# Optimization experiments

Measured on AMD Instinct MI355X. Metric: run time of the kernel, lower is better.

Reference implementation:

```python
import jax, jax.numpy as jnp
import numpy as np

MAX_POS = 100
N_NEGS = 10
B, L = 64, 100
VOCAB, WDIM, PDIM = 100000, 300, 50
N_TYPES, TDIM = 5000, 128
N_RELS, EDIM = 500, 128
N_FILTERS, FILTER_SIZES, EN_DIM = 128, (3, 5, 7), 512
N_POSS_C = 10
N_CANDS = N_POSS_C + N_NEGS
NB_PER_CAND = 64
N_NB = B * N_CANDS * NB_PER_CAND          # 81920 neighbor rows
TYPES_PER_NB = 4
T_TOTAL = N_NB * TYPES_PER_NB             # 327680 type entries
DIM = WDIM + PDIM                         # conv input width
CTX_DIM = len(FILTER_SIZES) * N_FILTERS * 2
EN_HID1 = CTX_DIM + EDIM                  # 896
NEG_INF = 1e10


def setup_inputs() -> dict:
    key = jax.random.key(0)
    ks = jax.random.split(key, 20)
    tokens = jax.random.randint(ks[0], (B, L), 0, VOCAB)
    pos_wrt_m = jax.random.randint(ks[1], (B, L), 0, 2 * MAX_POS + 1) - MAX_POS
    masks = jnp.ones((B, L), jnp.float32)
    nb_types = jax.random.randint(ks[2], (T_TOTAL,), 0, N_TYPES)
    nb_type_ids = jnp.arange(T_TOTAL) // TYPES_PER_NB      # each nb row gets TYPES_PER_NB types
    nb_n_types = jnp.full((N_NB,), TYPES_PER_NB, jnp.int32)
    nb_rs = jax.random.randint(ks[3], (N_NB,), 0, N_RELS)
    cand_nb_ids = jnp.arange(N_NB) // NB_PER_CAND          # each candidate gets NB_PER_CAND nbs
    real_n_poss = jax.random.randint(ks[4], (B,), 1, N_POSS_C + 1)
    we = jax.random.normal(ks[5], (VOCAB, WDIM), jnp.float32)
    word_embs = we / jnp.linalg.norm(we, axis=1, keepdims=True)  # F.normalize
    pos_emb_table = jax.random.normal(ks[6], (2 * MAX_POS + 1, PDIM), jnp.float32)
    type_emb_table = jax.random.normal(ks[7], (N_TYPES, TDIM), jnp.float32)
    rel_emb_table = jax.random.normal(ks[8], (N_RELS, EDIM), jnp.float32)
    rel_weight = jax.random.normal(ks[9], (TDIM, EDIM), jnp.float32) * np.sqrt(2.0 / EDIM)  # kaiming fan_out
    convs = {}
    for i, fs in enumerate(FILTER_SIZES):
        convs[f'conv_w{fs}'] = jax.random.normal(ks[10 + i], (N_FILTERS, 1, fs, DIM), jnp.float32) * np.sqrt(1.0 / (fs * DIM))
        convs[f'conv_b{fs}'] = jnp.zeros((N_FILTERS,), jnp.float32)
    scorer_W1 = jax.random.normal(ks[13], (EN_HID1, EN_DIM), jnp.float32) * np.sqrt(1.0 / EN_HID1)
    scorer_b1 = jnp.zeros((EN_DIM,), jnp.float32)
    scorer_W2 = jax.random.normal(ks[14], (EN_DIM, 1), jnp.float32) * np.sqrt(1.0 / EN_DIM)
    scorer_b2 = jnp.zeros((1,), jnp.float32)
    noise_W1 = jax.random.normal(ks[15], (EN_HID1, EN_DIM), jnp.float32) * np.sqrt(1.0 / EN_HID1)
    noise_b1 = jnp.zeros((EN_DIM,), jnp.float32)
    noise_W2 = jax.random.normal(ks[16], (EN_DIM, 1), jnp.float32) * np.sqrt(1.0 / EN_DIM)
    noise_b2 = jnp.zeros((1,), jnp.float32)
    return dict(tokens=tokens, pos_wrt_m=pos_wrt_m, masks=masks, nb_types=nb_types,
                nb_type_ids=nb_type_ids, nb_n_types=nb_n_types, nb_rs=nb_rs,
                cand_nb_ids=cand_nb_ids, real_n_poss=real_n_poss, n_poss=N_POSS_C,
                word_embs=word_embs, pos_emb_table=pos_emb_table,
                type_emb_table=type_emb_table, rel_emb_table=rel_emb_table,
                rel_weight=rel_weight, **convs,
                scorer_W1=scorer_W1, scorer_b1=scorer_b1, scorer_W2=scorer_W2, scorer_b2=scorer_b2,
                noise_W1=noise_W1, noise_b1=noise_b1, noise_W2=noise_W2, noise_b2=noise_b2)


def _mlp(x, W1, b1, W2, b2):
    return jax.nn.relu(x @ W1 + b1) @ W2 + b2


def _conv(x, w, b, fs):
    # x: [B,1,L,DIM], w: [nf,1,fs,DIM] -> [B,nf,L] (odd fs, 'same' padding on length)
    y = jax.lax.conv_general_dilated(x, w, window_strides=(1, 1),
                                     padding=[(fs // 2, fs // 2), (0, 0)],
                                     dimension_numbers=('NCHW', 'OIHW', 'NCHW'))
    return jax.nn.relu(y + b[None, :, None, None])[:, :, :, 0]


def _forward(tokens, pos_wrt_m, masks, nb_types, nb_type_ids, nb_n_types, nb_rs,
             cand_nb_ids, real_n_poss, n_poss, word_embs, pos_emb_table,
             type_emb_table, rel_emb_table, rel_weight,
             conv_w3, conv_b3, conv_w5, conv_b5, conv_w7, conv_b7,
             scorer_W1, scorer_b1, scorer_W2, scorer_b2,
             noise_W1, noise_b1, noise_W2, noise_b2):
    n_cands = n_poss + N_NEGS
    # --- neighbor type aggregation (TYPE_OPT == 'mean') ---
    nb_embs = jax.ops.segment_sum(type_emb_table[nb_types], nb_type_ids, num_segments=N_NB)
    nb_embs = nb_embs / nb_n_types[:, None].astype(jnp.float32)
    # --- relation transform + scatter_add into candidates ---
    msg = nb_embs @ rel_weight + rel_emb_table[nb_rs]                 # [N_NB, EDIM]
    cand_embs = jax.nn.relu(jax.ops.segment_sum(msg, cand_nb_ids, num_segments=B * n_cands))
    # --- PCNN context encoder ---
    pos_ment = pos_emb_table[pos_wrt_m + MAX_POS]                     # [B,L,PDIM]
    inp = jnp.concatenate([word_embs[tokens], pos_ment], axis=2)      # [B,L,DIM]
    x = inp[:, None, :, :]                                            # [B,1,L,DIM]
    conved = [_conv(x, conv_w3, conv_b3, 3), _conv(x, conv_w5, conv_b5, 5), _conv(x, conv_w7, conv_b7, 7)]
    ml = (pos_wrt_m <= 0).astype(jnp.float32)[:, None, :]             # [B,1,L]
    mr = ((pos_wrt_m >= 0).astype(jnp.float32) * masks)[:, None, :]
    pooled_l = jnp.concatenate([jnp.max(c * ml - (1.0 - ml) * NEG_INF, axis=2) for c in conved], axis=1)
    pooled_r = jnp.concatenate([jnp.max(c * mr - (1.0 - mr) * NEG_INF, axis=2) for c in conved], axis=1)
    ctx_vecs = jnp.concatenate([pooled_l, pooled_r], axis=1)          # [B, CTX_DIM]
    # --- scorer over (ctx, cand) pairs ---
    rp_ctx = jnp.broadcast_to(ctx_vecs[:, None, :], (B, n_cands, CTX_DIM)).reshape(B * n_cands, CTX_DIM)
    reprs = jnp.concatenate([rp_ctx, cand_embs], axis=1)
    scores = _mlp(reprs, scorer_W1, scorer_b1, scorer_W2, scorer_b2).reshape(B, n_cands)
    pos_mask = jnp.arange(1, n_poss + 1)[None, :] <= real_n_poss[:, None]
    mask = jnp.concatenate([pos_mask, jnp.ones((B, N_NEGS), bool)], axis=1)
    scores = jnp.where(mask, scores, -NEG_INF)
    # --- noise scorer over softmax-weighted positive candidate embedding ---
    p = jax.nn.softmax(scores[:, :n_poss], axis=-1)
    e = jnp.sum(cand_embs.reshape(B, n_cands, EDIM)[:, :n_poss, :] * p[:, :, None], axis=1)
    noise_scores = _mlp(jnp.concatenate([ctx_vecs, e], axis=1), noise_W1, noise_b1, noise_W2, noise_b2)
    return scores, noise_scores


def reference(tokens, pos_wrt_m, masks, nb_types, nb_type_ids, nb_n_types, nb_rs,
              cand_nb_ids, real_n_poss, n_poss, word_embs, pos_emb_table,
              type_emb_table, rel_emb_table, rel_weight,
              conv_w3, conv_b3, conv_w5, conv_b5, conv_w7, conv_b7,
              scorer_W1, scorer_b1, scorer_W2, scorer_b2,
              noise_W1, noise_b1, noise_W2, noise_b2):
    return _forward(tokens, pos_wrt_m, masks, nb_types, nb_type_ids, nb_n_types, nb_rs,
                    cand_nb_ids, real_n_poss, n_poss, word_embs, pos_emb_table,
                    type_emb_table, rel_emb_table, rel_weight,
                    conv_w3, conv_b3, conv_w5, conv_b5, conv_w7, conv_b7,
                    scorer_W1, scorer_b1, scorer_W2, scorer_b2,
                    noise_W1, noise_b1, noise_W2, noise_b2)


if __name__ == '__main__':
    out = reference(**setup_inputs())
    print(out[0].shape, out[1].shape)
```

## Files before the change

kernel.cpp:

```cpp
#include <hip/hip_runtime.h>
#include <hip/hip_bf16.h>

#define B 64
#define L 100
#define WDIM 300
#define PDIM 50
#define DIM 350
#define NK0 11
#define BRICK_ROWS 144
#define NSHIFT 7
#define NKK 77
#define N_CANDS 20
#define N_POSS 10
#define NB_PER_CAND 64
#define TDIM 128
#define EDIM 128
#define CTX_DIM 768
#define EN_HID1 896
#define EN_DIM 512
#define NEG_INF_F 1.0e10f

typedef __attribute__((ext_vector_type(8))) short bf16x8;
typedef __attribute__((ext_vector_type(4))) float f32x4;
typedef __attribute__((ext_vector_type(16))) float f32x16;

__device__ __forceinline__ void gload_lds16(const __hip_bfloat16* g,
                                            __hip_bfloat16* l) {
  __builtin_amdgcn_global_load_lds(
      (const __attribute__((address_space(1))) unsigned int*)(g),
      (__attribute__((address_space(3))) unsigned int*)(l), 16, 0, 0);
}

__device__ __forceinline__ bf16x8 cvt8(float4 a, float4 b) {
  union { bf16x8 v; __hip_bfloat16 h[8]; } u;
  u.h[0] = __float2bfloat16(a.x); u.h[1] = __float2bfloat16(a.y);
  u.h[2] = __float2bfloat16(a.z); u.h[3] = __float2bfloat16(a.w);
  u.h[4] = __float2bfloat16(b.x); u.h[5] = __float2bfloat16(b.y);
  u.h[6] = __float2bfloat16(b.z); u.h[7] = __float2bfloat16(b.w);
  return u.v;
}

__global__ __launch_bounds__(256) void k_front(
    const int* __restrict__ nb_types, const int* __restrict__ nb_n_types,
    const int* __restrict__ nb_rs, const float* __restrict__ type_emb,
    const float* __restrict__ rel_emb, const float* __restrict__ rel_weight,
    __hip_bfloat16* __restrict__ candb, const int* __restrict__ tokens,
    const int* __restrict__ pos, const float* __restrict__ word_embs,
    const float* __restrict__ pos_emb, __hip_bfloat16* __restrict__ Xbr,
    const float* __restrict__ w3, const float* __restrict__ w5,
    const float* __restrict__ w7, __hip_bfloat16* __restrict__ Wbr,
    const float* __restrict__ sW1, const float* __restrict__ nW1,
    __hip_bfloat16* __restrict__ W1br, float* __restrict__ ctxpool) {
  int blk = blockIdx.x, tid = threadIdx.x;
  __shared__ int sty[NB_PER_CAND * 4];
  __shared__ int srs[NB_PER_CAND];
  __shared__ float sinv[NB_PER_CAND];
  __shared__ float pS[2][128], pR[2][128], sS[128];
  __shared__ float tile[112][33];

  if (blk < 1280) {
    int c = blk;
    int g = tid >> 7, d = tid & 127;
    sty[tid] = nb_types[c * NB_PER_CAND * 4 + tid];
    if (tid < NB_PER_CAND) {
      srs[tid] = nb_rs[c * NB_PER_CAND + tid];
      sinv[tid] = 1.f / (float)nb_n_types[c * NB_PER_CAND + tid];
    }
    __syncthreads();
    float accS = 0.f, accR = 0.f;
#pragma unroll 4
    for (int j2 = 0; j2 < 32; ++j2) {
      int j = g * 32 + j2;
      accR += rel_emb[srs[j] * EDIM + d];
      float s4 = 0.f;
#pragma unroll
      for (int k = 0; k < 4; ++k) s4 += type_emb[sty[j * 4 + k] * TDIM + d];
      accS = fmaf(s4, sinv[j], accS);
    }
    pS[g][d] = accS;
    pR[g][d] = accR;
    __syncthreads();
    if (tid < 128) sS[d] = pS[0][d] + pS[1][d];
    __syncthreads();
    float dotp = (g == 0) ? (pR[0][d] + pR[1][d]) : 0.f;
#pragma unroll 4
    for (int k2 = 0; k2 < 64; ++k2) {
      int k = g * 64 + k2;
      dotp = fmaf(sS[k], rel_weight[k * EDIM + d], dotp);
    }
    pS[g][d] = dotp;
    __syncthreads();
    if (tid < 128)
      candb[(size_t)c * EDIM + d] =
          __float2bfloat16(fmaxf(pS[0][d] + pS[1][d], 0.f));
  } else if (blk < 2432) {
    int idx = blk - 1280;
    int b = idx / 18, r0 = (idx % 18) * 8;
    __hip_bfloat16* base = Xbr + (size_t)b * (NK0 * BRICK_ROWS * 32);
    for (int r = r0; r < r0 + 8; ++r) {
      int lp = r - 3;
      int xr = (r >> 1) & 3;
      if (lp >= 0 && lp < L) {
        int tok = tokens[b * L + lp];
        int pp = pos[b * L + lp] + 100;
        const float* wrow = word_embs + (size_t)tok * WDIM;
        const float* prow = pos_emb + (size_t)pp * PDIM;
        for (int d = tid; d < 352; d += 256) {
          float v = (d < WDIM) ? wrow[d] : (d < DIM) ? prow[d - WDIM] : 0.f;
          int slot = (d >> 3) & 3;
          base[((size_t)(d >> 5) * BRICK_ROWS + r) * 32 +
               ((slot ^ xr) << 3) + (d & 7)] = __float2bfloat16(v);
        }
      } else {
        for (int d = tid; d < 352; d += 256) {
          int slot = (d >> 3) & 3;
          base[((size_t)(d >> 5) * BRICK_ROWS + r) * 32 +
               ((slot ^ xr) << 3) + (d & 7)] = __float2bfloat16(0.f);
        }
      }
    }
  } else if (blk < 2663) {
    int idx = blk - 2432;
    int ncg = idx / NKK, kkb = idx % NKK;
    if (tid < 128) {
      int k0 = kkb / NSHIFT, s = kkb - NSHIFT * k0;
      int col = tid;
      const float* w = (ncg == 0) ? w3 : (ncg == 1) ? w5 : w7;
      int fs = (ncg == 0) ? 3 : (ncg == 1) ? 5 : 7;
      int dl = (ncg == 0) ? s - 2 : (ncg == 1) ? s - 1 : s;
      bool valid = (dl >= 0 && dl < fs);
      __hip_bfloat16* dst = Wbr + (((size_t)ncg * NKK + kkb) * 128 + col) * 32;
      for (int k = 0; k < 32; ++k) {
        int d = k0 * 32 + k;
        float v =
            (valid && d < DIM) ? w[((size_t)col * fs + dl) * DIM + d] : 0.f;
        dst[k] = __float2bfloat16(v);
      }
    }
  } else if (blk < 2919) {
    int idx = blk - 2663;
    int which = idx >> 7;
    int rem = idx & 127;
    int sub = rem >> 3;
    int kc = rem & 7;
    const float* src = which ? nW1 : sW1;
    __hip_bfloat16* dst = W1br + (size_t)which * (16 * 56 * 512);
    for (int i = tid; i < 112 * 32; i += 256) {
      int kk = i >> 5, col = i & 31;
      tile[kk][col] = src[(size_t)(kc * 112 + kk) * EN_DIM + sub * 32 + col];
    }
    __syncthreads();
    for (int i = tid; i < 32 * 112; i += 256) {
      int col = i / 112, kk = i - col * 112;
      int k = kc * 112 + kk;
      dst[((size_t)(sub * 56 + (k >> 4)) * 32 + col) * 16 + (k & 15)] =
          __float2bfloat16(tile[kk][col]);
    }
  } else {
    int idx = blk - 2919;
    int i0 = idx * 1024 + tid * 4;
#pragma unroll
    for (int q = 0; q < 4; ++q) ctxpool[i0 + q] = -NEG_INF_F;
  }
}

__global__ __launch_bounds__(256) void k_conv(
    const __hip_bfloat16* __restrict__ Xbr,
    const __hip_bfloat16* __restrict__ Wbr, const int* __restrict__ pos,
    const float* __restrict__ masks, const float* __restrict__ b3,
    const float* __restrict__ b5, const float* __restrict__ b7,
    float* __restrict__ ctxpool) {
  int b = blockIdx.x;
  int mt = blockIdx.y;
  int nt = blockIdx.z;
  int ncg = nt >> 1, nh = nt & 1;
  int slo = 2 - ncg, shi = 4 + ncg;
  int tid = threadIdx.x;
  int wv = tid >> 6, ln = tid & 63;
  int wm = wv >> 1, wn = wv & 1;
  int l15 = ln & 15, kg = ln >> 4;

  __shared__ __align__(16) __hip_bfloat16 Asb[2][80 * 32];
  __shared__ float sml[64], smr[64];

  if (tid < 64) {
    int l = mt * 64 + tid;
    float mlv = 0.f, mrv = 0.f;
    if (l < L) {
      int p = pos[b * L + l];
      mlv = (p <= 0) ? 1.f : 0.f;
      mrv = (p >= 0) ? masks[b * L + l] : 0.f;
    }
    sml[tid] = mlv;
    smr[tid] = mrv;
  }

  const __hip_bfloat16* XB =
      Xbr + (size_t)b * (NK0 * BRICK_ROWS * 32) + (size_t)mt * 64 * 32;
  const __hip_bfloat16* WBl =
      Wbr + ((size_t)ncg * NKK * 128 + nh * 64 + wn * 32 + l15) * 32 + kg * 8;

  for (int seg = wv; seg < 5; seg += 4)
    gload_lds16(XB + (seg * 64 + ln) * 8, &Asb[0][(seg * 64 + ln) * 8]);
  __syncthreads();

  f32x4 acc[2][2];
#pragma unroll
  for (int i = 0; i < 2; ++i)
#pragma unroll
    for (int j = 0; j < 2; ++j) acc[i][j] = (f32x4){0.f, 0.f, 0.f, 0.f};

  int buf = 0;
  for (int k0 = 0; k0 < NK0; ++k0) {
    if (k0 < NK0 - 1) {
      const __hip_bfloat16* asrc = XB + (size_t)(k0 + 1) * (BRICK_ROWS * 32);
      for (int seg = wv; seg < 5; seg += 4)
        gload_lds16(asrc + (seg * 64 + ln) * 8,
                    &Asb[buf ^ 1][(seg * 64 + ln) * 8]);
    }
#pragma unroll
    for (int s = 0; s < NSHIFT; ++s) {
      if (s < slo || s > shi) continue;
      const __hip_bfloat16* bp = WBl + (size_t)(k0 * NSHIFT + s) * 4096;
      bf16x8 bf0 = *(const bf16x8*)(bp);
      bf16x8 bf1 = *(const bf16x8*)(bp + 512);
      int rbase = wm * 32 + l15 + s;
      int xr = (kg ^ ((rbase >> 1) & 3)) << 3;
      bf16x8 af0 = *(const bf16x8*)&Asb[buf][rbase * 32 + xr];
      bf16x8 af1 = *(const bf16x8*)&Asb[buf][(rbase + 16) * 32 + xr];
      acc[0][0] = __builtin_amdgcn_mfma_f32_16x16x32_bf16(af0, bf0, acc[0][0], 0, 0, 0);
      acc[0][1] = __builtin_amdgcn_mfma_f32_16x16x32_bf16(af0, bf1, acc[0][1], 0, 0, 0);
      acc[1][0] = __builtin_amdgcn_mfma_f32_16x16x32_bf16(af1, bf0, acc[1][0], 0, 0, 0);
      acc[1][1] = __builtin_amdgcn_mfma_f32_16x16x32_bf16(af1, bf1, acc[1][1], 0, 0, 0);
    }
    __syncthreads();
    buf ^= 1;
  }

  const float* barr = (ncg == 0) ? b3 : (ncg == 1) ? b5 : b7;
#pragma unroll
  for (int j = 0; j < 2; ++j) {
    int fcol = nh * 64 + wn * 32 + 16 * j + l15;
    float bias = barr[fcol];
    float mpl = -NEG_INF_F, mpr = -NEG_INF_F;
#pragma unroll
    for (int i = 0; i < 2; ++i) {
#pragma unroll
      for (int r = 0; r < 4; ++r) {
        int rl = wm * 32 + 16 * i + 4 * kg + r;
        float cva = fmaxf(acc[i][j][r] + bias, 0.f);
        float ml = sml[rl], mr = smr[rl];
        mpl = fmaxf(mpl, cva * ml - (1.f - ml) * NEG_INF_F);
        mpr = fmaxf(mpr, cva * mr - (1.f - mr) * NEG_INF_F);
      }
    }
    mpl = fmaxf(mpl, __shfl_xor(mpl, 16));
    mpl = fmaxf(mpl, __shfl_xor(mpl, 32));
    mpr = fmaxf(mpr, __shfl_xor(mpr, 16));
    mpr = fmaxf(mpr, __shfl_xor(mpr, 32));
    if (ln < 16) {
      atomicMax((int*)&ctxpool[(size_t)b * CTX_DIM + ncg * 128 + fcol],
                __float_as_int(mpl));
      atomicMax((int*)&ctxpool[(size_t)b * CTX_DIM + 384 + ncg * 128 + fcol],
                __float_as_int(mpr));
    }
  }
}

__global__ __launch_bounds__(128) void k_mlp(
    const float* __restrict__ ctxp, const __hip_bfloat16* __restrict__ candb,
    const __hip_bfloat16* __restrict__ W1br, const float* __restrict__ sb1,
    const float* __restrict__ sW2, float* __restrict__ part,
    float* __restrict__ hctxn) {
  int mt = blockIdx.x;
  bool noise = (mt >= 40);
  int w = threadIdx.x >> 6;
  int sub = blockIdx.y * 2 + w;
  int lane = threadIdx.x & 63;
  int lrow = lane & 31, kg2 = lane >> 5;
  __shared__ __align__(16) __hip_bfloat16 As[32 * 904];

  {
    int row = threadIdx.x >> 2, seg = threadIdx.x & 3;
    int xr = (row >> 1) & 7;
    if (!noise) {
      int m = mt * 32 + row;
      int bb = m / 20;
      const float* cp = ctxp + (size_t)bb * CTX_DIM;
#pragma unroll
      for (int q = 0; q < 28; ++q) {
        int k = seg * 224 + q * 8;
        bf16x8 v;
        if (k < CTX_DIM)
          v = cvt8(*(const float4*)(cp + k), *(const float4*)(cp + k + 4));
        else
          v = *(const bf16x8*)&candb[(size_t)m * EDIM + (k - CTX_DIM)];
        *(bf16x8*)&As[row * 904 + (((k >> 3) ^ xr) << 3)] = v;
      }
    } else {
      int bb = (mt - 40) * 32 + row;
      const float* cp = ctxp + (size_t)bb * CTX_DIM;
#pragma unroll
      for (int q = 0; q < 28; ++q) {
        int k = seg * 224 + q * 8;
        if (k < CTX_DIM)
          *(bf16x8*)&As[row * 904 + (((k >> 3) ^ xr) << 3)] =
              cvt8(*(const float4*)(cp + k), *(const float4*)(cp + k + 4));
      }
    }
  }
  __syncthreads();

  int xrr = (lrow >> 1) & 7;
  f32x16 acc = {};
  if (!noise) {
    const __hip_bfloat16* W1b = W1br;
#pragma unroll 4
    for (int k0 = 0; k0 < 56; ++k0) {
      int s16 = k0 * 2 + kg2;
      bf16x8 av = *(const bf16x8*)&As[lrow * 904 + ((s16 ^ xrr) << 3)];
      bf16x8 bv = *(const bf16x8*)&W1b[((size_t)sub * 56 + k0) * 512 +
                                       lrow * 16 + kg2 * 8];
      acc = __builtin_amdgcn_mfma_f32_32x32x16_bf16(av, bv, acc, 0, 0, 0);
    }
    int n = sub * 32 + lrow;
    float b1n = sb1[n], w2n = sW2[n];
#pragma unroll
    for (int r = 0; r < 16; ++r) {
      float v = fmaxf(acc[r] + b1n, 0.f) * w2n;
#pragma unroll
      for (int off = 16; off; off >>= 1) v += __shfl_xor(v, off);
      if (lrow == 0) {
        int mm = mt * 32 + (r & 3) + 8 * (r >> 2) + 4 * kg2;
        part[(size_t)sub * (B * N_CANDS) + mm] = v;
      }
    }
  } else {
    const __hip_bfloat16* W1b = W1br + (size_t)(16 * 56 * 512);
#pragma unroll 4
    for (int k0 = 0; k0 < 48; ++k0) {
      int s16 = k0 * 2 + kg2;
      bf16x8 av = *(const bf16x8*)&As[lrow * 904 + ((s16 ^ xrr) << 3)];
      bf16x8 bv = *(const bf16x8*)&W1b[((size_t)sub * 56 + k0) * 512 +
                                       lrow * 16 + kg2 * 8];
      acc = __builtin_amdgcn_mfma_f32_32x32x16_bf16(av, bv, acc, 0, 0, 0);
    }
#pragma unroll
    for (int r = 0; r < 16; ++r) {
      int mrow = (r & 3) + 8 * (r >> 2) + 4 * kg2;
      hctxn[(size_t)((mt - 40) * 32 + mrow) * EN_DIM + sub * 32 + lrow] =
          acc[r];
    }
  }
}

__global__ __launch_bounds__(256) void k_tail(
    const float* __restrict__ part, const __hip_bfloat16* __restrict__ candb,
    const float* __restrict__ hctxn, const int* __restrict__ real_n_poss,
    const float* __restrict__ sb2, const float* __restrict__ nW1,
    const float* __restrict__ nb1, const float* __restrict__ nW2,
    const float* __restrict__ nb2, float* __restrict__ out) {
  int b = blockIdx.x, tid = threadIdx.x;
  __shared__ float ssc[N_CANDS];
  __shared__ float sp[N_POSS];
  __shared__ float e_sh[EDIM];
  __shared__ float red[4];

  if (tid < N_CANDS) {
    int m = b * N_CANDS + tid;
    float s = sb2[0];
#pragma unroll
    for (int p = 0; p < 16; ++p) s += part[(size_t)p * (B * N_CANDS) + m];
    if (tid < N_POSS && (tid + 1) > real_n_poss[b]) s = -NEG_INF_F;
    ssc[tid] = s;
    out[m] = s;
  }
  __syncthreads();
  if (tid == 0) {
    float mx = -INFINITY;
#pragma unroll
    for (int c = 0; c < N_POSS; ++c) mx = fmaxf(mx, ssc[c]);
    float ssum = 0.f;
    float pe[N_POSS];
#pragma unroll
    for (int c = 0; c < N_POSS; ++c) {
      pe[c] = expf(ssc[c] - mx);
      ssum += pe[c];
    }
    float inv = 1.f / ssum;
#pragma unroll
    for (int c = 0; c < N_POSS; ++c) sp[c] = pe[c] * inv;
  }
  __syncthreads();
  if (tid < EDIM) {
    float ev = 0.f;
#pragma unroll
    for (int c = 0; c < N_POSS; ++c)
      ev = fmaf(sp[c],
                __bfloat162float(candb[(size_t)(b * N_CANDS + c) * EDIM + tid]),
                ev);
    e_sh[tid] = ev;
  }
  __syncthreads();

  float h0 = nb1[tid] + hctxn[(size_t)b * EN_DIM + tid];
  float h1 = nb1[tid + 256] + hctxn[(size_t)b * EN_DIM + tid + 256];
#pragma unroll 4
  for (int k = 0; k < EDIM; ++k) {
    float ek = e_sh[k];
    const float* wr = nW1 + (size_t)(CTX_DIM + k) * EN_DIM;
    h0 = fmaf(ek, wr[tid], h0);
    h1 = fmaf(ek, wr[tid + 256], h1);
  }
  float v = fmaxf(h0, 0.f) * nW2[tid] + fmaxf(h1, 0.f) * nW2[tid + 256];
#pragma unroll
  for (int off = 32; off; off >>= 1) v += __shfl_xor(v, off);
  if ((tid & 63) == 0) red[tid >> 6] = v;
  __syncthreads();
  if (tid == 0)
    out[B * N_CANDS + b] = red[0] + red[1] + red[2] + red[3] + nb2[0];
}

extern "C" void kernel_launch(void* const* d_in, const int* in_sizes, int n_in,
                              void* d_out, int out_size, void* d_ws,
                              size_t ws_size, hipStream_t stream) {
  const int* tokens = (const int*)d_in[0];
  const int* pos = (const int*)d_in[1];
  const float* masks = (const float*)d_in[2];
  const int* nb_types = (const int*)d_in[3];
  const int* nb_n_types = (const int*)d_in[5];
  const int* nb_rs = (const int*)d_in[6];
  const int* real_n_poss = (const int*)d_in[8];
  const float* word_embs = (const float*)d_in[10];
  const float* pos_emb = (const float*)d_in[11];
  const float* type_emb = (const float*)d_in[12];
  const float* rel_emb = (const float*)d_in[13];
  const float* rel_weight = (const float*)d_in[14];
  const float* w3 = (const float*)d_in[15];
  const float* b3 = (const float*)d_in[16];
  const float* w5 = (const float*)d_in[17];
  const float* b5 = (const float*)d_in[18];
  const float* w7 = (const float*)d_in[19];
  const float* b7 = (const float*)d_in[20];
  const float* sW1 = (const float*)d_in[21];
  const float* sb1 = (const float*)d_in[22];
  const float* sW2 = (const float*)d_in[23];
  const float* sb2 = (const float*)d_in[24];
  const float* nW1 = (const float*)d_in[25];
  const float* nb1 = (const float*)d_in[26];
  const float* nW2 = (const float*)d_in[27];
  const float* nb2 = (const float*)d_in[28];

  __hip_bfloat16* Xbr = (__hip_bfloat16*)d_ws;
  __hip_bfloat16* Wbr = Xbr + (size_t)3244032;
  __hip_bfloat16* W1br = Wbr + (size_t)946176;
  __hip_bfloat16* candb = W1br + (size_t)917504;
  float* ctxpool = (float*)(candb + (size_t)163840);
  float* part = ctxpool + (size_t)B * CTX_DIM;
  float* hctxn = part + (size_t)16 * B * N_CANDS;
  float* out = (float*)d_out;

  hipLaunchKernelGGL(k_front, dim3(2967), dim3(256), 0, stream, nb_types,
                     nb_n_types, nb_rs, type_emb, rel_emb, rel_weight, candb,
                     tokens, pos, word_embs, pos_emb, Xbr, w3, w5, w7, Wbr,
                     sW1, nW1, W1br, ctxpool);
  hipLaunchKernelGGL(k_conv, dim3(B, 2, 6), dim3(256), 0, stream, Xbr, Wbr,
                     pos, masks, b3, b5, b7, ctxpool);
  hipLaunchKernelGGL(k_mlp, dim3(42, 8), dim3(128), 0, stream, ctxpool, candb,
                     W1br, sb1, sW2, part, hctxn);
  hipLaunchKernelGGL(k_tail, dim3(B), dim3(256), 0, stream, part, candb,
                     hctxn, real_n_poss, sb2, nW1, nb1, nW2, nb2, out);
}
```

Baseline: 94.97 us.

## Move candidate embedding and W1 repack work into the conv kernel launch

The candidate-embedding reduction and the MLP weight repack move out of the front kernel into a new combined kernel that also runs the conv blocks. The front kernel now only builds the conv inputs and weights and initialises the pool, so it is shorter, and the moved independent work runs alongside the conv tiles in one launch. This cuts one kernel's serialized tail and lets the memory-bound gather overlap the MFMA conv. The cost is a heterogeneous grid with a shared-memory union, where long conv blocks and short gather blocks compete for the same slots.

```diff
diff --git a/kernel.cpp b/kernel.cpp
--- a/kernel.cpp
+++ b/kernel.cpp
@@ -41,60 +41,14 @@
 }
 
 __global__ __launch_bounds__(256) void k_front(
-    const int* __restrict__ nb_types, const int* __restrict__ nb_n_types,
-    const int* __restrict__ nb_rs, const float* __restrict__ type_emb,
-    const float* __restrict__ rel_emb, const float* __restrict__ rel_weight,
-    __hip_bfloat16* __restrict__ candb, const int* __restrict__ tokens,
-    const int* __restrict__ pos, const float* __restrict__ word_embs,
-    const float* __restrict__ pos_emb, __hip_bfloat16* __restrict__ Xbr,
-    const float* __restrict__ w3, const float* __restrict__ w5,
-    const float* __restrict__ w7, __hip_bfloat16* __restrict__ Wbr,
-    const float* __restrict__ sW1, const float* __restrict__ nW1,
-    __hip_bfloat16* __restrict__ W1br, float* __restrict__ ctxpool) {
+    const int* __restrict__ tokens, const int* __restrict__ pos,
+    const float* __restrict__ word_embs, const float* __restrict__ pos_emb,
+    __hip_bfloat16* __restrict__ Xbr, const float* __restrict__ w3,
+    const float* __restrict__ w5, const float* __restrict__ w7,
+    __hip_bfloat16* __restrict__ Wbr, float* __restrict__ ctxpool) {
   int blk = blockIdx.x, tid = threadIdx.x;
-  __shared__ int sty[NB_PER_CAND * 4];
-  __shared__ int srs[NB_PER_CAND];
-  __shared__ float sinv[NB_PER_CAND];
-  __shared__ float pS[2][128], pR[2][128], sS[128];
-  __shared__ float tile[112][33];
-
-  if (blk < 1280) {
-    int c = blk;
-    int g = tid >> 7, d = tid & 127;
-    sty[tid] = nb_types[c * NB_PER_CAND * 4 + tid];
-    if (tid < NB_PER_CAND) {
-      srs[tid] = nb_rs[c * NB_PER_CAND + tid];
-      sinv[tid] = 1.f / (float)nb_n_types[c * NB_PER_CAND + tid];
-    }
-    __syncthreads();
-    float accS = 0.f, accR = 0.f;
-#pragma unroll 4
-    for (int j2 = 0; j2 < 32; ++j2) {
-      int j = g * 32 + j2;
-      accR += rel_emb[srs[j] * EDIM + d];
-      float s4 = 0.f;
-#pragma unroll
-      for (int k = 0; k < 4; ++k) s4 += type_emb[sty[j * 4 + k] * TDIM + d];
-      accS = fmaf(s4, sinv[j], accS);
-    }
-    pS[g][d] = accS;
-    pR[g][d] = accR;
-    __syncthreads();
-    if (tid < 128) sS[d] = pS[0][d] + pS[1][d];
-    __syncthreads();
-    float dotp = (g == 0) ? (pR[0][d] + pR[1][d]) : 0.f;
-#pragma unroll 4
-    for (int k2 = 0; k2 < 64; ++k2) {
-      int k = g * 64 + k2;
-      dotp = fmaf(sS[k], rel_weight[k * EDIM + d], dotp);
-    }
-    pS[g][d] = dotp;
-    __syncthreads();
-    if (tid < 128)
-      candb[(size_t)c * EDIM + d] =
-          __float2bfloat16(fmaxf(pS[0][d] + pS[1][d], 0.f));
-  } else if (blk < 2432) {
-    int idx = blk - 1280;
+  if (blk < 1152) {
+    int idx = blk;
     int b = idx / 18, r0 = (idx % 18) * 8;
     __hip_bfloat16* base = Xbr + (size_t)b * (NK0 * BRICK_ROWS * 32);
     for (int r = r0; r < r0 + 8; ++r) {
@@ -119,8 +73,8 @@
         }
       }
     }
-  } else if (blk < 2663) {
-    int idx = blk - 2432;
+  } else if (blk < 1383) {
+    int idx = blk - 1152;
     int ncg = idx / NKK, kkb = idx % NKK;
     if (tid < 128) {
       int k0 = kkb / NSHIFT, s = kkb - NSHIFT * k0;
@@ -137,132 +91,187 @@
         dst[k] = __float2bfloat16(v);
       }
     }
-  } else if (blk < 2919) {
-    int idx = blk - 2663;
+  } else {
+    int idx = blk - 1383;
+    int i0 = idx * 1024 + tid * 4;
+#pragma unroll
+    for (int q = 0; q < 4; ++q) ctxpool[i0 + q] = -NEG_INF_F;
+  }
+}
+
+__global__ __launch_bounds__(256) void k_work(
+    const __hip_bfloat16* __restrict__ Xbr,
+    const __hip_bfloat16* __restrict__ Wbr, const int* __restrict__ pos,
+    const float* __restrict__ masks, const float* __restrict__ b3,
+    const float* __restrict__ b5, const float* __restrict__ b7,
+    float* __restrict__ ctxpool, const int* __restrict__ nb_types,
+    const int* __restrict__ nb_n_types, const int* __restrict__ nb_rs,
+    const float* __restrict__ type_emb, const float* __restrict__ rel_emb,
+    const float* __restrict__ rel_weight, __hip_bfloat16* __restrict__ candb,
+    const float* __restrict__ sW1, const float* __restrict__ nW1,
+    __hip_bfloat16* __restrict__ W1br) {
+  __shared__ __align__(16) char smem[14848];
+  int blk = blockIdx.x, tid = threadIdx.x;
+
+  if (blk < 768) {
+    int idx = blk;
+    int b = idx / 12;
+    int rem = idx - b * 12;
+    int mt = rem / 6, nt = rem - mt * 6;
+    int ncg = nt >> 1, nh = nt & 1;
+    int slo = 2 - ncg, shi = 4 + ncg;
+    int wv = tid >> 6, ln = tid & 63;
+    int wm = wv >> 1, wn = wv & 1;
+    int l15 = ln & 15, kg = ln >> 4;
+
+    __hip_bfloat16* Asb = (__hip_bfloat16*)smem;
+    float* sml = (float*)(smem + 10240);
+    float* smr = (float*)(smem + 10496);
+
+    if (tid < 64) {
+      int l = mt * 64 + tid;
+      float mlv = 0.f, mrv = 0.f;
+      if (l < L) {
+        int p = pos[b * L + l];
+        mlv = (p <= 0) ? 1.f : 0.f;
+        mrv = (p >= 0) ? masks[b * L + l] : 0.f;
+      }
+      sml[tid] = mlv;
+      smr[tid] = mrv;
+    }
+
+    const __hip_bfloat16* XB =
+        Xbr + (size_t)b * (NK0 * BRICK_ROWS * 32) + (size_t)mt * 64 * 32;
+    const __hip_bfloat16* WBl =
+        Wbr + ((size_t)ncg * NKK * 128 + nh * 64 + wn * 32 + l15) * 32 +
+        kg * 8;
+
+    for (int seg = wv; seg < 5; seg += 4)
+      gload_lds16(XB + (seg * 64 + ln) * 8, &Asb[(seg * 64 + ln) * 8]);
+    __syncthreads();
+
+    f32x4 acc[2][2];
+#pragma unroll
+    for (int i = 0; i < 2; ++i)
+#pragma unroll
+      for (int j = 0; j < 2; ++j) acc[i][j] = (f32x4){0.f, 0.f, 0.f, 0.f};
+
+    int buf = 0;
+    for (int k0 = 0; k0 < NK0; ++k0) {
+      if (k0 < NK0 - 1) {
+        const __hip_bfloat16* asrc = XB + (size_t)(k0 + 1) * (BRICK_ROWS * 32);
+        for (int seg = wv; seg < 5; seg += 4)
+          gload_lds16(asrc + (seg * 64 + ln) * 8,
+                      &Asb[(buf ^ 1) * 2560 + (seg * 64 + ln) * 8]);
+      }
+#pragma unroll
+      for (int s = 0; s < NSHIFT; ++s) {
+        if (s < slo || s > shi) continue;
+        const __hip_bfloat16* bp = WBl + (size_t)(k0 * NSHIFT + s) * 4096;
+        bf16x8 bf0 = *(const bf16x8*)(bp);
+        bf16x8 bf1 = *(const bf16x8*)(bp + 512);
+        int rbase = wm * 32 + l15 + s;
+        int xr = (kg ^ ((rbase >> 1) & 3)) << 3;
+        bf16x8 af0 = *(const bf16x8*)&Asb[buf * 2560 + rbase * 32 + xr];
+        bf16x8 af1 = *(const bf16x8*)&Asb[buf * 2560 + (rbase + 16) * 32 + xr];
+        acc[0][0] = __builtin_amdgcn_mfma_f32_16x16x32_bf16(af0, bf0, acc[0][0], 0, 0, 0);
+        acc[0][1] = __builtin_amdgcn_mfma_f32_16x16x32_bf16(af0, bf1, acc[0][1], 0, 0, 0);
+        acc[1][0] = __builtin_amdgcn_mfma_f32_16x16x32_bf16(af1, bf0, acc[1][0], 0, 0, 0);
+        acc[1][1] = __builtin_amdgcn_mfma_f32_16x16x32_bf16(af1, bf1, acc[1][1], 0, 0, 0);
+      }
+      __syncthreads();
+      buf ^= 1;
+    }
+
+    const float* barr = (ncg == 0) ? b3 : (ncg == 1) ? b5 : b7;
+#pragma unroll
+    for (int j = 0; j < 2; ++j) {
+      int fcol = nh * 64 + wn * 32 + 16 * j + l15;
+      float bias = barr[fcol];
+      float mpl = -NEG_INF_F, mpr = -NEG_INF_F;
+#pragma unroll
+      for (int i = 0; i < 2; ++i) {
+#pragma unroll
+        for (int r = 0; r < 4; ++r) {
+          int rl = wm * 32 + 16 * i + 4 * kg + r;
+          float cva = fmaxf(acc[i][j][r] + bias, 0.f);
+          float ml = sml[rl], mr = smr[rl];
+          mpl = fmaxf(mpl, cva * ml - (1.f - ml) * NEG_INF_F);
+          mpr = fmaxf(mpr, cva * mr - (1.f - mr) * NEG_INF_F);
+        }
+      }
+      mpl = fmaxf(mpl, __shfl_xor(mpl, 16));
+      mpl = fmaxf(mpl, __shfl_xor(mpl, 32));
+      mpr = fmaxf(mpr, __shfl_xor(mpr, 16));
+      mpr = fmaxf(mpr, __shfl_xor(mpr, 32));
+      if (ln < 16) {
+        atomicMax((int*)&ctxpool[(size_t)b * CTX_DIM + ncg * 128 + fcol],
+                  __float_as_int(mpl));
+        atomicMax((int*)&ctxpool[(size_t)b * CTX_DIM + 384 + ncg * 128 + fcol],
+                  __float_as_int(mpr));
+      }
+    }
+  } else if (blk < 2048) {
+    int c = blk - 768;
+    int g = tid >> 7, d = tid & 127;
+    int* sty = (int*)smem;
+    int* srs = (int*)(smem + 1024);
+    float* sinv = (float*)(smem + 1280);
+    float* pS = (float*)(smem + 1536);
+    float* pR = (float*)(smem + 2560);
+    float* sS = (float*)(smem + 3584);
+    sty[tid] = nb_types[c * NB_PER_CAND * 4 + tid];
+    if (tid < NB_PER_CAND) {
+      srs[tid] = nb_rs[c * NB_PER_CAND + tid];
+      sinv[tid] = 1.f / (float)nb_n_types[c * NB_PER_CAND + tid];
+    }
+    __syncthreads();
+    float accS = 0.f, accR = 0.f;
+#pragma unroll 4
+    for (int j2 = 0; j2 < 32; ++j2) {
+      int j = g * 32 + j2;
+      accR += rel_emb[srs[j] * EDIM + d];
+      float s4 = 0.f;
+#pragma unroll
+      for (int k = 0; k < 4; ++k) s4 += type_emb[sty[j * 4 + k] * TDIM + d];
+      accS = fmaf(s4, sinv[j], accS);
+    }
+    pS[g * 128 + d] = accS;
+    pR[g * 128 + d] = accR;
+    __syncthreads();
+    if (tid < 128) sS[d] = pS[d] + pS[128 + d];
+    __syncthreads();
+    float dotp = (g == 0) ? (pR[d] + pR[128 + d]) : 0.f;
+#pragma unroll 4
+    for (int k2 = 0; k2 < 64; ++k2) {
+      int k = g * 64 + k2;
+      dotp = fmaf(sS[k], rel_weight[k * EDIM + d], dotp);
+    }
+    pS[g * 128 + d] = dotp;
+    __syncthreads();
+    if (tid < 128)
+      candb[(size_t)c * EDIM + d] =
+          __float2bfloat16(fmaxf(pS[d] + pS[128 + d], 0.f));
+  } else {
+    int idx = blk - 2048;
     int which = idx >> 7;
     int rem = idx & 127;
     int sub = rem >> 3;
     int kc = rem & 7;
+    float* tile = (float*)smem;
     const float* src = which ? nW1 : sW1;
     __hip_bfloat16* dst = W1br + (size_t)which * (16 * 56 * 512);
     for (int i = tid; i < 112 * 32; i += 256) {
       int kk = i >> 5, col = i & 31;
-      tile[kk][col] = src[(size_t)(kc * 112 + kk) * EN_DIM + sub * 32 + col];
+      tile[kk * 33 + col] =
+          src[(size_t)(kc * 112 + kk) * EN_DIM + sub * 32 + col];
     }
     __syncthreads();
     for (int i = tid; i < 32 * 112; i += 256) {
       int col = i / 112, kk = i - col * 112;
       int k = kc * 112 + kk;
       dst[((size_t)(sub * 56 + (k >> 4)) * 32 + col) * 16 + (k & 15)] =
-          __float2bfloat16(tile[kk][col]);
-    }
-  } else {
-    int idx = blk - 2919;
-    int i0 = idx * 1024 + tid * 4;
-#pragma unroll
-    for (int q = 0; q < 4; ++q) ctxpool[i0 + q] = -NEG_INF_F;
-  }
-}
-
-__global__ __launch_bounds__(256) void k_conv(
-    const __hip_bfloat16* __restrict__ Xbr,
-    const __hip_bfloat16* __restrict__ Wbr, const int* __restrict__ pos,
-    const float* __restrict__ masks, const float* __restrict__ b3,
-    const float* __restrict__ b5, const float* __restrict__ b7,
-    float* __restrict__ ctxpool) {
-  int b = blockIdx.x;
-  int mt = blockIdx.y;
-  int nt = blockIdx.z;
-  int ncg = nt >> 1, nh = nt & 1;
-  int slo = 2 - ncg, shi = 4 + ncg;
-  int tid = threadIdx.x;
-  int wv = tid >> 6, ln = tid & 63;
-  int wm = wv >> 1, wn = wv & 1;
-  int l15 = ln & 15, kg = ln >> 4;
-
-  __shared__ __align__(16) __hip_bfloat16 Asb[2][80 * 32];
-  __shared__ float sml[64], smr[64];
-
-  if (tid < 64) {
-    int l = mt * 64 + tid;
-    float mlv = 0.f, mrv = 0.f;
-    if (l < L) {
-      int p = pos[b * L + l];
-      mlv = (p <= 0) ? 1.f : 0.f;
-      mrv = (p >= 0) ? masks[b * L + l] : 0.f;
-    }
-    sml[tid] = mlv;
-    smr[tid] = mrv;
-  }
-
-  const __hip_bfloat16* XB =
-      Xbr + (size_t)b * (NK0 * BRICK_ROWS * 32) + (size_t)mt * 64 * 32;
-  const __hip_bfloat16* WBl =
-      Wbr + ((size_t)ncg * NKK * 128 + nh * 64 + wn * 32 + l15) * 32 + kg * 8;
-
-  for (int seg = wv; seg < 5; seg += 4)
-    gload_lds16(XB + (seg * 64 + ln) * 8, &Asb[0][(seg * 64 + ln) * 8]);
-  __syncthreads();
-
-  f32x4 acc[2][2];
-#pragma unroll
-  for (int i = 0; i < 2; ++i)
-#pragma unroll
-    for (int j = 0; j < 2; ++j) acc[i][j] = (f32x4){0.f, 0.f, 0.f, 0.f};
-
-  int buf = 0;
-  for (int k0 = 0; k0 < NK0; ++k0) {
-    if (k0 < NK0 - 1) {
-      const __hip_bfloat16* asrc = XB + (size_t)(k0 + 1) * (BRICK_ROWS * 32);
-      for (int seg = wv; seg < 5; seg += 4)
-        gload_lds16(asrc + (seg * 64 + ln) * 8,
-                    &Asb[buf ^ 1][(seg * 64 + ln) * 8]);
-    }
-#pragma unroll
-    for (int s = 0; s < NSHIFT; ++s) {
-      if (s < slo || s > shi) continue;
-      const __hip_bfloat16* bp = WBl + (size_t)(k0 * NSHIFT + s) * 4096;
-      bf16x8 bf0 = *(const bf16x8*)(bp);
-      bf16x8 bf1 = *(const bf16x8*)(bp + 512);
-      int rbase = wm * 32 + l15 + s;
-      int xr = (kg ^ ((rbase >> 1) & 3)) << 3;
-      bf16x8 af0 = *(const bf16x8*)&Asb[buf][rbase * 32 + xr];
-      bf16x8 af1 = *(const bf16x8*)&Asb[buf][(rbase + 16) * 32 + xr];
-      acc[0][0] = __builtin_amdgcn_mfma_f32_16x16x32_bf16(af0, bf0, acc[0][0], 0, 0, 0);
-      acc[0][1] = __builtin_amdgcn_mfma_f32_16x16x32_bf16(af0, bf1, acc[0][1], 0, 0, 0);
-      acc[1][0] = __builtin_amdgcn_mfma_f32_16x16x32_bf16(af1, bf0, acc[1][0], 0, 0, 0);
-      acc[1][1] = __builtin_amdgcn_mfma_f32_16x16x32_bf16(af1, bf1, acc[1][1], 0, 0, 0);
-    }
-    __syncthreads();
-    buf ^= 1;
-  }
-
-  const float* barr = (ncg == 0) ? b3 : (ncg == 1) ? b5 : b7;
-#pragma unroll
-  for (int j = 0; j < 2; ++j) {
-    int fcol = nh * 64 + wn * 32 + 16 * j + l15;
-    float bias = barr[fcol];
-    float mpl = -NEG_INF_F, mpr = -NEG_INF_F;
-#pragma unroll
-    for (int i = 0; i < 2; ++i) {
-#pragma unroll
-      for (int r = 0; r < 4; ++r) {
-        int rl = wm * 32 + 16 * i + 4 * kg + r;
-        float cva = fmaxf(acc[i][j][r] + bias, 0.f);
-        float ml = sml[rl], mr = smr[rl];
-        mpl = fmaxf(mpl, cva * ml - (1.f - ml) * NEG_INF_F);
-        mpr = fmaxf(mpr, cva * mr - (1.f - mr) * NEG_INF_F);
-      }
-    }
-    mpl = fmaxf(mpl, __shfl_xor(mpl, 16));
-    mpl = fmaxf(mpl, __shfl_xor(mpl, 32));
-    mpr = fmaxf(mpr, __shfl_xor(mpr, 16));
-    mpr = fmaxf(mpr, __shfl_xor(mpr, 32));
-    if (ln < 16) {
-      atomicMax((int*)&ctxpool[(size_t)b * CTX_DIM + ncg * 128 + fcol],
-                __float_as_int(mpl));
-      atomicMax((int*)&ctxpool[(size_t)b * CTX_DIM + 384 + ncg * 128 + fcol],
-                __float_as_int(mpr));
+          __float2bfloat16(tile[kk * 33 + col]);
     }
   }
 }
@@ -460,12 +469,11 @@
   float* hctxn = part + (size_t)16 * B * N_CANDS;
   float* out = (float*)d_out;
 
-  hipLaunchKernelGGL(k_front, dim3(2967), dim3(256), 0, stream, nb_types,
-                     nb_n_types, nb_rs, type_emb, rel_emb, rel_weight, candb,
-                     tokens, pos, word_embs, pos_emb, Xbr, w3, w5, w7, Wbr,
-                     sW1, nW1, W1br, ctxpool);
-  hipLaunchKernelGGL(k_conv, dim3(B, 2, 6), dim3(256), 0, stream, Xbr, Wbr,
-                     pos, masks, b3, b5, b7, ctxpool);
+  hipLaunchKernelGGL(k_front, dim3(1431), dim3(256), 0, stream, tokens, pos,
+                     word_embs, pos_emb, Xbr, w3, w5, w7, Wbr, ctxpool);
+  hipLaunchKernelGGL(k_work, dim3(2304), dim3(256), 0, stream, Xbr, Wbr, pos,
+                     masks, b3, b5, b7, ctxpool, nb_types, nb_n_types, nb_rs,
+                     type_emb, rel_emb, rel_weight, candb, sW1, nW1, W1br);
   hipLaunchKernelGGL(k_mlp, dim3(42, 8), dim3(128), 0, stream, ctxpool, candb,
                      W1br, sb1, sW2, part, hctxn);
   hipLaunchKernelGGL(k_tail, dim3(B), dim3(256), 0, stream, part, candb,
```

After: 84.41 us. -11.1%, faster.
